# Performance work log

Hardware: AMD Instinct MI355X
Metric: run time of the kernel (lower is better)

## Reference

```python
import jax
import jax.numpy as jnp
import numpy as np

B, L = 64, 128


def _lse(x, axis):
    # -inf-safe logsumexp; mirrors the torch code's NaN-masking autograd hooks
    m = jax.lax.stop_gradient(jnp.max(x, axis=axis, keepdims=True))
    m = jnp.where(jnp.isfinite(m), m, 0.0)
    s = jnp.sum(jnp.exp(x - m), axis=axis)
    out = jnp.log(jnp.where(s > 0, s, 1.0)) + jnp.squeeze(m, axis=axis)
    return jnp.where(s > 0, out, -jnp.inf)


def _inside(scores_p, lens):
    # scores_p: [L, L, B] == torch scores.permute(2, 1, 0); Eisner inside algorithm
    L_, _, Bn = scores_p.shape
    ar = jnp.arange(L_)
    ninf = jnp.array(-jnp.inf, scores_p.dtype)
    s_i = jnp.full((L_, L_, Bn), -jnp.inf, scores_p.dtype)  # incomplete spans
    s_c = jnp.full((L_, L_, Bn), -jnp.inf, scores_p.dtype)  # complete spans
    s_c = s_c.at[ar, ar].set(0.0)

    def step(carry, w):
        s_i, s_c = carry
        i = ar[:, None]                      # span start
        j = ar[None, :]                      # split offset
        valid = (j < w) & (i < L_ - w)       # [L, L] stripe mask for width w
        clip = lambda x: jnp.clip(x, 0, L_ - 1)
        vi = (ar < L_ - w)[:, None]          # valid span starts, [L, 1]
        lo, hi = clip(ar + w), ar            # diagonal coords (i+w, i)

        # incomplete: I(i<->i+w) = lse_r C(i, i+r) + C(i+w, i+r+1)  (stripe + stripe(w,1))
        ilr = s_c[clip(i), clip(i + j)] + s_c[clip(i + w), clip(i + j + 1)]
        il = _lse(jnp.where(valid[..., None], ilr, ninf), 1)       # [L, B]
        s_i = s_i.at[lo, hi].set(jnp.where(vi, il + scores_p[lo, hi], s_i[lo, hi]))
        s_i = s_i.at[hi, lo].set(jnp.where(vi, il + scores_p[hi, lo], s_i[hi, lo]))

        # complete left: C(i+w -> i) = lse_r C(i+r, i) + I(i+w, i+r)
        cl = s_c[clip(i + j), clip(i)] + s_i[clip(i + w), clip(i + j)]
        clv = _lse(jnp.where(valid[..., None], cl, ninf), 1)
        s_c = s_c.at[lo, hi].set(jnp.where(vi, clv, s_c[lo, hi]))

        # complete right: C(i -> i+w) = lse_r I(i, i+r+1) + C(i+r+1, i+w)
        cr = s_i[clip(i), clip(i + j + 1)] + s_c[clip(i + j + 1), clip(i + w)]
        crv = _lse(jnp.where(valid[..., None], cr, ninf), 1)
        # root span (0, w) is only valid for sentences of exactly length w
        crv = crv.at[0].set(jnp.where(lens == w, crv[0], ninf))
        s_c = s_c.at[hi, lo].set(jnp.where(vi, crv, s_c[hi, lo]))
        return (s_i, s_c), None

    (s_i, s_c), _ = jax.lax.scan(jax.checkpoint(step), (s_i, s_c), jnp.arange(1, L_))
    return s_i, s_c


def setup_inputs() -> dict:
    key = jax.random.key(0)
    k1, k2, k3 = jax.random.split(key, 3)
    scores = jax.random.normal(k1, (B, L, L), jnp.float32)
    lens = jax.random.randint(k2, (B,), L // 2, L)                 # sentence lengths
    pos = jnp.arange(L)
    mask = (pos[None, :] >= 1) & (pos[None, :] <= lens[:, None])   # prefix mask, mask.sum(1)==lens
    target = jax.random.randint(k3, (B, L), 0, L)
    target = jnp.minimum(target, lens[:, None])                    # gold heads inside sentence
    return {"scores": scores, "mask": mask, "target": target}


def reference(scores, mask, target):
    Bn, L_, _ = scores.shape
    lens = mask.sum(1)
    total = mask.sum().astype(scores.dtype)
    s_i, s_c = _inside(jnp.transpose(scores, (2, 1, 0)), lens)
    logZ = s_c[0, lens, jnp.arange(Bn)].sum()
    gold = jnp.take_along_axis(scores, target[..., None], axis=-1)[..., 0]
    loss = (logZ - jnp.where(mask, gold, jnp.zeros((), scores.dtype)).sum()) / total
    return loss
```

## Files before the change

kernel.cpp:

```cpp
#include <hip/hip_runtime.h>
#include <math.h>

#define LL 128
#define LP 129
#define TCR 144
#define TC_SZ (TCR * LP)
#define TI_SZ (LL * LP + 160)
#define NT 512
#define NW 8

#define LOG2E 1.4426950408889634f
#define LN2   0.6931471805599453f

template <int CTRL>
__device__ __forceinline__ float dppq(float v) {
  return __int_as_float(__builtin_amdgcn_update_dpp(
      0, __float_as_int(v), CTRL, 0xF, 0xF, true));
}
__device__ __forceinline__ float qmax(float v) {
  v = fmaxf(v, dppq<0xB1>(v));
  v = fmaxf(v, dppq<0x4E>(v));
  return v;
}
__device__ __forceinline__ float qsum(float v) {
  v += dppq<0xB1>(v);
  v += dppq<0x4E>(v);
  return v;
}
template <int MASK>
__device__ __forceinline__ float swz(float v) {
  return __int_as_float(__builtin_amdgcn_ds_swizzle(
      __float_as_int(v), (MASK << 10) | 0x1F));
}
template <int G>
__device__ __forceinline__ float gmaxr(float v) {
  v = qmax(v);
  if constexpr (G >= 8)  v = fmaxf(v, swz<4>(v));
  if constexpr (G >= 16) v = fmaxf(v, swz<8>(v));
  if constexpr (G >= 32) v = fmaxf(v, swz<16>(v));
  return v;
}
template <int G>
__device__ __forceinline__ float gsumr(float v) {
  v = qsum(v);
  if constexpr (G >= 8)  v += swz<4>(v);
  if constexpr (G >= 16) v += swz<8>(v);
  if constexpr (G >= 32) v += swz<16>(v);
  return v;
}

template <int K>
__device__ __forceinline__ void fusedPhase(
    float* __restrict__ tC, float* __restrict__ tI, const float* __restrict__ S,
    const int ii, const int w, const int jg, const bool writer,
    const bool rootBad, float (&paR)[17], float (&a1R)[17], float (&c1R)[17]) {
  const float sUp = S[ii * LL + ii + w];
  const float sLo = S[(ii + w) * LL + ii];
  const float* pb = tC + (ii + w) * LP + ii + 1 + jg;
  const float* a2 = tI + (ii + w) * LP + ii + jg;
  const float* c2 = tC + (ii + 1 + jg) * LP + ii + w;

  float vb[K], va[K], vc[K];
#pragma unroll
  for (int k = 0; k < K; ++k) vb[k] = pb[4 * k];
#pragma unroll
  for (int k = 0; k < K; ++k) va[k] = a2[4 * k];
#pragma unroll
  for (int k = 0; k < K; ++k) vc[k] = c2[4 * k * LP];

  float mA0 = -INFINITY, mA1 = -INFINITY;
#pragma unroll
  for (int k = 0; k < K; ++k) {
    float x = paR[k] + vb[k];
    if (k & 1) mA1 = fmaxf(mA1, x); else mA0 = fmaxf(mA0, x);
  }
  const float msA = fmaxf(qmax(fmaxf(mA0, mA1)), -1e37f);
  const float nA = -msA * LOG2E;
  float sA0 = 0.f, sA1 = 0.f;
#pragma unroll
  for (int k = 0; k < K; ++k) {
    float e = __builtin_amdgcn_exp2f(__builtin_fmaf(paR[k] + vb[k], LOG2E, nA));
    if (k & 1) sA1 += e; else sA0 += e;
  }
  const float il = __builtin_amdgcn_logf(qsum(sA0 + sA1)) * LN2 + msA;

  float mL0 = -INFINITY, mL1 = -INFINITY;
#pragma unroll
  for (int k = 0; k < K; ++k) {
    float x = a1R[k] + va[k];
    if (k & 1) mL1 = fmaxf(mL1, x); else mL0 = fmaxf(mL0, x);
  }
  const float mL = qmax(fmaxf(mL0, mL1));
  const float msL = fmaxf(mL, -1e37f);
  const float nL = -msL * LOG2E;
  float sL0 = 0.f, sL1 = 0.f;
#pragma unroll
  for (int k = 0; k < K; ++k) {
    float e = __builtin_amdgcn_exp2f(__builtin_fmaf(a1R[k] + va[k], LOG2E, nL));
    if (k & 1) sL1 += e; else sL0 += e;
  }
  const float SL = qsum(sL0 + sL1);

  float mR0 = -INFINITY, mR1 = -INFINITY;
#pragma unroll
  for (int k = 0; k < K; ++k) {
    float x = c1R[k] + vc[k];
    if (k & 1) mR1 = fmaxf(mR1, x); else mR0 = fmaxf(mR0, x);
  }
  const float mR = qmax(fmaxf(mR0, mR1));
  const float msR = fmaxf(mR, -1e37f);
  const float nR = -msR * LOG2E;
  float sR0 = 0.f, sR1 = 0.f;
#pragma unroll
  for (int k = 0; k < K; ++k) {
    float e = __builtin_amdgcn_exp2f(__builtin_fmaf(c1R[k] + vc[k], LOG2E, nR));
    if (k & 1) sR1 += e; else sR0 += e;
  }
  const float SR = qsum(sR0 + sR1);

  const float t0 = il + sUp;
  const float tW = il + sLo;
  const float msfL = fmaxf(fmaxf(mL, t0), -1e37f);
  const float SLf = SL * __builtin_amdgcn_exp2f((msL - msfL) * LOG2E)
                  + __builtin_amdgcn_exp2f((t0 - msfL) * LOG2E);
  const float clv = __builtin_amdgcn_logf(SLf) * LN2 + msfL;
  const float msfR = fmaxf(fmaxf(mR, tW), -1e37f);
  const float SRf = SR * __builtin_amdgcn_exp2f((msR - msfR) * LOG2E)
                  + __builtin_amdgcn_exp2f((tW - msfR) * LOG2E);
  float crv = __builtin_amdgcn_logf(SRf) * LN2 + msfR;
  if (rootBad) crv = -INFINITY;

  if (writer) {
    tI[(ii + w) * LP + ii] = t0;
    tI[ii * LP + (ii + w)] = tW;
    tC[(ii + w) * LP + ii] = clv;
    tC[ii * LP + (ii + w)] = crv;
  }

  const int wm3 = w & 3;
  const bool lnw = (jg == wm3) && (wm3 != 0);
  paR[K - 1] = lnw ? crv : paR[K - 1];
  a1R[K - 1] = lnw ? clv : a1R[K - 1];
  if constexpr (K < 16) {
    const bool z = (jg == 0) && (wm3 == 0);
    paR[K] = z ? crv : paR[K];
    a1R[K] = z ? clv : a1R[K];
  } else {
    const bool z = (jg == 0) && (wm3 == 0);
    paR[16] = z ? crv : paR[16];
    a1R[16] = z ? clv : a1R[16];
  }
  const bool ln1 = (jg == ((w - 1) & 3));
  c1R[K - 1] = ln1 ? tW : c1R[K - 1];
}

template <int G, int KG>
__device__ __forceinline__ void widePhase(
    float* __restrict__ tC, float* __restrict__ tI, const float* __restrict__ S,
    const int ii, const int w, const int jgg, const bool writer,
    const bool rootBad) {
  const float sUp = S[ii * LL + ii + w];
  const float sLo = S[(ii + w) * LL + ii];
  const float* pa = tC + ii * LP + ii + jgg;
  const float* pb = tC + (ii + w) * LP + ii + 1 + jgg;
  const float* a1 = tC + (ii + jgg) * LP + ii;
  const float* a2 = tI + (ii + w) * LP + ii + jgg;
  const float* c1 = tI + ii * LP + ii + 1 + jgg;
  const float* c2 = tC + (ii + 1 + jgg) * LP + ii + w;

  float xa[KG], xl[KG], xr[KG];
  const unsigned uw = (unsigned)w, uw1 = (unsigned)(w - 1);
#pragma unroll
  for (int k = 0; k < KG; ++k) {
    float va_ = pa[G * k] + pb[G * k];
    float vl_ = a1[G * k * LP] + a2[G * k];
    float vr_ = c1[G * k] + c2[G * k * LP];
    const unsigned j = (unsigned)(jgg + G * k);
    xa[k] = (j < uw) ? va_ : -INFINITY;
    xl[k] = (j - 1u < uw1) ? vl_ : -INFINITY;
    xr[k] = (j < uw1) ? vr_ : -INFINITY;
  }

  float mA0 = -INFINITY, mA1 = -INFINITY;
#pragma unroll
  for (int k = 0; k < KG; ++k) {
    if (k & 1) mA1 = fmaxf(mA1, xa[k]); else mA0 = fmaxf(mA0, xa[k]);
  }
  const float msA = fmaxf(gmaxr<G>(fmaxf(mA0, mA1)), -1e37f);
  const float nA = -msA * LOG2E;
  float sA0 = 0.f, sA1 = 0.f;
#pragma unroll
  for (int k = 0; k < KG; ++k) {
    float e = __builtin_amdgcn_exp2f(__builtin_fmaf(xa[k], LOG2E, nA));
    if (k & 1) sA1 += e; else sA0 += e;
  }
  const float il = __builtin_amdgcn_logf(gsumr<G>(sA0 + sA1)) * LN2 + msA;

  float mL0 = -INFINITY, mL1 = -INFINITY;
#pragma unroll
  for (int k = 0; k < KG; ++k) {
    if (k & 1) mL1 = fmaxf(mL1, xl[k]); else mL0 = fmaxf(mL0, xl[k]);
  }
  const float mL = gmaxr<G>(fmaxf(mL0, mL1));
  const float msL = fmaxf(mL, -1e37f);
  const float nL = -msL * LOG2E;
  float sL0 = 0.f, sL1 = 0.f;
#pragma unroll
  for (int k = 0; k < KG; ++k) {
    float e = __builtin_amdgcn_exp2f(__builtin_fmaf(xl[k], LOG2E, nL));
    if (k & 1) sL1 += e; else sL0 += e;
  }
  const float SL = gsumr<G>(sL0 + sL1);

  float mR0 = -INFINITY, mR1 = -INFINITY;
#pragma unroll
  for (int k = 0; k < KG; ++k) {
    if (k & 1) mR1 = fmaxf(mR1, xr[k]); else mR0 = fmaxf(mR0, xr[k]);
  }
  const float mR = gmaxr<G>(fmaxf(mR0, mR1));
  const float msR = fmaxf(mR, -1e37f);
  const float nR = -msR * LOG2E;
  float sR0 = 0.f, sR1 = 0.f;
#pragma unroll
  for (int k = 0; k < KG; ++k) {
    float e = __builtin_amdgcn_exp2f(__builtin_fmaf(xr[k], LOG2E, nR));
    if (k & 1) sR1 += e; else sR0 += e;
  }
  const float SR = gsumr<G>(sR0 + sR1);

  const float t0 = il + sUp;
  const float tW = il + sLo;
  const float msfL = fmaxf(fmaxf(mL, t0), -1e37f);
  const float SLf = SL * __builtin_amdgcn_exp2f((msL - msfL) * LOG2E)
                  + __builtin_amdgcn_exp2f((t0 - msfL) * LOG2E);
  const float clv = __builtin_amdgcn_logf(SLf) * LN2 + msfL;
  const float msfR = fmaxf(fmaxf(mR, tW), -1e37f);
  const float SRf = SR * __builtin_amdgcn_exp2f((msR - msfR) * LOG2E)
                  + __builtin_amdgcn_exp2f((tW - msfR) * LOG2E);
  float crv = __builtin_amdgcn_logf(SRf) * LN2 + msfR;
  if (rootBad) crv = -INFINITY;

  if (writer) {
    tI[(ii + w) * LP + ii] = t0;
    tI[ii * LP + (ii + w)] = tW;
    tC[(ii + w) * LP + ii] = clv;
    tC[ii * LP + (ii + w)] = crv;
  }
}

__global__ __launch_bounds__(NT, 2) void crf_inside(
    const float* __restrict__ scores, const int* __restrict__ mask,
    const int* __restrict__ target, float* __restrict__ acc) {
  extern __shared__ float lds[];
  float* tC = lds;
  float* tI = lds + TC_SZ;
  const int b = blockIdx.x;
  const int t = threadIdx.x;
  const int lane = t & 63;
  const int wv = t >> 6;
  const int r = lane >> 2;
  const int jg = lane & 3;
  const float* S = scores + (size_t)b * LL * LL;

  __shared__ float gred[NW];
  __shared__ int lred[NW];
  __shared__ float s_gold;
  __shared__ int s_len;

  int mv = 0; float gv = 0.f;
  if (t < LL) {
    mv = mask[b * LL + t] ? 1 : 0;
    if (mv) gv = S[t * LL + target[b * LL + t]];
  }
  int lm = mv; float lg = gv;
#pragma unroll
  for (int o = 32; o > 0; o >>= 1) {
    lm += __shfl_xor(lm, o, 64);
    lg += __shfl_xor(lg, o, 64);
  }
  if (lane == 0) { lred[wv] = lm; gred[wv] = lg; }

  for (int idx = t; idx < TC_SZ + TI_SZ; idx += NT) lds[idx] = -INFINITY;
  __syncthreads();
  if (t < LL) tC[t * LP + t] = 0.f;
  if (t == 0) {
    int l = 0; float g = 0.f;
    for (int k = 0; k < NW; ++k) { l += lred[k]; g += gred[k]; }
    s_len = l; s_gold = g;
  }
  __syncthreads();
  const int len = s_len;

  const int i = (wv << 4) + r;

  float paR[17], a1R[17], c1R[17];
#pragma unroll
  for (int k = 0; k < 17; ++k) { paR[k] = -INFINITY; a1R[k] = -INFINITY; c1R[k] = -INFINITY; }
  if (jg == 0) paR[0] = 0.f;

  for (int w = 1; w <= 64; ++w) {
    const int ni = LL - w;
    const bool waveAct = (wv << 4) < ni;
    const int ii = min(i, ni - 1);
    const bool writer = (jg == 0) & (i < ni);
    const bool rootBad = (ii == 0) && (w != len);
    const int K = (w + 3) >> 2;
    if (waveAct) {
      switch (K) {
#define CASE_K(KK) case KK: fusedPhase<KK>(tC, tI, S, ii, w, jg, writer, rootBad, paR, a1R, c1R); break;
        CASE_K(1) CASE_K(2) CASE_K(3) CASE_K(4) CASE_K(5) CASE_K(6)
        CASE_K(7) CASE_K(8) CASE_K(9) CASE_K(10) CASE_K(11) CASE_K(12)
        CASE_K(13) CASE_K(14) CASE_K(15) CASE_K(16)
#undef CASE_K
      }
    }
    __syncthreads();
  }

  for (int w = 65; w < LL; ++w) {
    const int ni = LL - w;
    if (w <= 96) {
      const int gi = t >> 3, jgg = t & 7;
      if ((wv << 3) < ni) {
        const int ii = min(gi, ni - 1);
        const bool writer = (jgg == 0) & (gi < ni);
        const bool rootBad = (ii == 0) && (w != len);
        switch ((w + 7) >> 3) {
          case 9:  widePhase<8, 9>(tC, tI, S, ii, w, jgg, writer, rootBad); break;
          case 10: widePhase<8, 10>(tC, tI, S, ii, w, jgg, writer, rootBad); break;
          case 11: widePhase<8, 11>(tC, tI, S, ii, w, jgg, writer, rootBad); break;
          default: widePhase<8, 12>(tC, tI, S, ii, w, jgg, writer, rootBad); break;
        }
      }
    } else if (w <= 112) {
      const int gi = t >> 4, jgg = t & 15;
      if ((wv << 2) < ni) {
        const int ii = min(gi, ni - 1);
        const bool writer = (jgg == 0) & (gi < ni);
        const bool rootBad = (ii == 0) && (w != len);
        widePhase<16, 7>(tC, tI, S, ii, w, jgg, writer, rootBad);
      }
    } else {
      const int gi = t >> 5, jgg = t & 31;
      if ((wv << 1) < ni) {
        const int ii = min(gi, ni - 1);
        const bool writer = (jgg == 0) & (gi < ni);
        const bool rootBad = (ii == 0) && (w != len);
        widePhase<32, 4>(tC, tI, S, ii, w, jgg, writer, rootBad);
      }
    }
    __syncthreads();
  }

  if (t == 0) {
    float logZ = tC[len];
    atomicAdd(&acc[0], logZ - s_gold);
    atomicAdd(&acc[1], (float)len);
  }
}

__global__ void zero_acc(float* acc) {
  acc[0] = 0.f;
  acc[1] = 0.f;
}

__global__ void finalize(const float* __restrict__ acc, float* __restrict__ out) {
  out[0] = acc[0] / acc[1];
}

extern "C" void kernel_launch(void* const* d_in, const int* in_sizes, int n_in,
                              void* d_out, int out_size, void* d_ws, size_t ws_size,
                              hipStream_t stream) {
  const float* scores = (const float*)d_in[0];
  const int* mask = (const int*)d_in[1];
  const int* target = (const int*)d_in[2];
  float* out = (float*)d_out;
  float* acc = (float*)d_ws;

  const int Bn = in_sizes[0] / (LL * LL);
  const size_t lds_bytes = (size_t)(TC_SZ + TI_SZ) * sizeof(float);

  (void)hipFuncSetAttribute((const void*)crf_inside,
                            hipFuncAttributeMaxDynamicSharedMemorySize,
                            (int)lds_bytes);

  zero_acc<<<1, 1, 0, stream>>>(acc);
  crf_inside<<<Bn, NT, lds_bytes, stream>>>(scores, mask, target, acc);
  finalize<<<1, 1, 0, stream>>>(acc, out);
}
```

Measured before the change: 267.6 us.

## Double block to 1024 threads with 8-lane span groups and wider reductions

```diff
diff --git a/kernel.cpp b/kernel.cpp
--- a/kernel.cpp
+++ b/kernel.cpp
@@ -2,12 +2,12 @@
 #include <math.h>
 
 #define LL 128
-#define LP 129
-#define TCR 144
+#define LP 132
+#define TCR 160
 #define TC_SZ (TCR * LP)
-#define TI_SZ (LL * LP + 160)
-#define NT 512
-#define NW 8
+#define TI_SZ (LL * LP + 48)
+#define NT 1024
+#define NW 16
 
 #define LOG2E 1.4426950408889634f
 #define LN2   0.6931471805599453f
@@ -17,24 +17,27 @@
   return __int_as_float(__builtin_amdgcn_update_dpp(
       0, __float_as_int(v), CTRL, 0xF, 0xF, true));
 }
-__device__ __forceinline__ float qmax(float v) {
-  v = fmaxf(v, dppq<0xB1>(v));
-  v = fmaxf(v, dppq<0x4E>(v));
-  return v;
-}
-__device__ __forceinline__ float qsum(float v) {
-  v += dppq<0xB1>(v);
-  v += dppq<0x4E>(v);
-  return v;
-}
 template <int MASK>
 __device__ __forceinline__ float swz(float v) {
   return __int_as_float(__builtin_amdgcn_ds_swizzle(
       __float_as_int(v), (MASK << 10) | 0x1F));
 }
+__device__ __forceinline__ float g8max(float v) {
+  v = fmaxf(v, dppq<0xB1>(v));
+  v = fmaxf(v, dppq<0x4E>(v));
+  v = fmaxf(v, dppq<0x141>(v));
+  return v;
+}
+__device__ __forceinline__ float g8sum(float v) {
+  v += dppq<0xB1>(v);
+  v += dppq<0x4E>(v);
+  v += dppq<0x141>(v);
+  return v;
+}
 template <int G>
 __device__ __forceinline__ float gmaxr(float v) {
-  v = qmax(v);
+  v = fmaxf(v, dppq<0xB1>(v));
+  v = fmaxf(v, dppq<0x4E>(v));
   if constexpr (G >= 8)  v = fmaxf(v, swz<4>(v));
   if constexpr (G >= 16) v = fmaxf(v, swz<8>(v));
   if constexpr (G >= 32) v = fmaxf(v, swz<16>(v));
@@ -42,7 +45,8 @@
 }
 template <int G>
 __device__ __forceinline__ float gsumr(float v) {
-  v = qsum(v);
+  v += dppq<0xB1>(v);
+  v += dppq<0x4E>(v);
   if constexpr (G >= 8)  v += swz<4>(v);
   if constexpr (G >= 16) v += swz<8>(v);
   if constexpr (G >= 32) v += swz<16>(v);
@@ -52,21 +56,20 @@
 template <int K>
 __device__ __forceinline__ void fusedPhase(
     float* __restrict__ tC, float* __restrict__ tI, const float* __restrict__ S,
-    const int ii, const int w, const int jg, const bool writer,
-    const bool rootBad, float (&paR)[17], float (&a1R)[17], float (&c1R)[17]) {
+    const int ii, const int w, const int lg, const bool writer,
+    const bool rootBad, float (&paR)[9], float (&a1R)[9], float (&c1R)[8]) {
   const float sUp = S[ii * LL + ii + w];
   const float sLo = S[(ii + w) * LL + ii];
-  const float* pb = tC + (ii + w) * LP + ii + 1 + jg;
-  const float* a2 = tI + (ii + w) * LP + ii + jg;
-  const float* c2 = tC + (ii + 1 + jg) * LP + ii + w;
-
-  float vb[K], va[K], vc[K];
-#pragma unroll
-  for (int k = 0; k < K; ++k) vb[k] = pb[4 * k];
-#pragma unroll
-  for (int k = 0; k < K; ++k) va[k] = a2[4 * k];
-#pragma unroll
-  for (int k = 0; k < K; ++k) vc[k] = c2[4 * k * LP];
+  const float* pb = tC + (ii + w) * LP + ii + 1 + lg;
+  const float* a2 = tI + (ii + w) * LP + ii + lg;
+  const float* c2 = tC + (ii + 1 + lg) * LP + ii + w;
+
+  float vb[K], va[K];
+#pragma unroll
+  for (int k = 0; k < K; ++k) vb[k] = pb[8 * k];
+#pragma unroll
+  for (int k = 0; k < K; ++k) va[k] = a2[8 * k];
+  __builtin_amdgcn_sched_barrier(0);
 
   float mA0 = -INFINITY, mA1 = -INFINITY;
 #pragma unroll
@@ -74,7 +77,7 @@
     float x = paR[k] + vb[k];
     if (k & 1) mA1 = fmaxf(mA1, x); else mA0 = fmaxf(mA0, x);
   }
-  const float msA = fmaxf(qmax(fmaxf(mA0, mA1)), -1e37f);
+  const float msA = fmaxf(g8max(fmaxf(mA0, mA1)), -1e37f);
   const float nA = -msA * LOG2E;
   float sA0 = 0.f, sA1 = 0.f;
 #pragma unroll
@@ -82,7 +85,7 @@
     float e = __builtin_amdgcn_exp2f(__builtin_fmaf(paR[k] + vb[k], LOG2E, nA));
     if (k & 1) sA1 += e; else sA0 += e;
   }
-  const float il = __builtin_amdgcn_logf(qsum(sA0 + sA1)) * LN2 + msA;
+  const float il = __builtin_amdgcn_logf(g8sum(sA0 + sA1)) * LN2 + msA;
 
   float mL0 = -INFINITY, mL1 = -INFINITY;
 #pragma unroll
@@ -90,7 +93,7 @@
     float x = a1R[k] + va[k];
     if (k & 1) mL1 = fmaxf(mL1, x); else mL0 = fmaxf(mL0, x);
   }
-  const float mL = qmax(fmaxf(mL0, mL1));
+  const float mL = g8max(fmaxf(mL0, mL1));
   const float msL = fmaxf(mL, -1e37f);
   const float nL = -msL * LOG2E;
   float sL0 = 0.f, sL1 = 0.f;
@@ -99,7 +102,12 @@
     float e = __builtin_amdgcn_exp2f(__builtin_fmaf(a1R[k] + va[k], LOG2E, nL));
     if (k & 1) sL1 += e; else sL0 += e;
   }
-  const float SL = qsum(sL0 + sL1);
+  const float SL = g8sum(sL0 + sL1);
+
+  float vc[K];
+#pragma unroll
+  for (int k = 0; k < K; ++k) vc[k] = c2[8 * k * LP];
+  __builtin_amdgcn_sched_barrier(0);
 
   float mR0 = -INFINITY, mR1 = -INFINITY;
 #pragma unroll
@@ -107,7 +115,7 @@
     float x = c1R[k] + vc[k];
     if (k & 1) mR1 = fmaxf(mR1, x); else mR0 = fmaxf(mR0, x);
   }
-  const float mR = qmax(fmaxf(mR0, mR1));
+  const float mR = g8max(fmaxf(mR0, mR1));
   const float msR = fmaxf(mR, -1e37f);
   const float nR = -msR * LOG2E;
   float sR0 = 0.f, sR1 = 0.f;
@@ -116,7 +124,7 @@
     float e = __builtin_amdgcn_exp2f(__builtin_fmaf(c1R[k] + vc[k], LOG2E, nR));
     if (k & 1) sR1 += e; else sR0 += e;
   }
-  const float SR = qsum(sR0 + sR1);
+  const float SR = g8sum(sR0 + sR1);
 
   const float t0 = il + sUp;
   const float tW = il + sLo;
@@ -137,20 +145,16 @@
     tC[ii * LP + (ii + w)] = crv;
   }
 
-  const int wm3 = w & 3;
-  const bool lnw = (jg == wm3) && (wm3 != 0);
+  const int wm7 = w & 7;
+  const bool lnw = (lg == wm7) && (wm7 != 0);
   paR[K - 1] = lnw ? crv : paR[K - 1];
   a1R[K - 1] = lnw ? clv : a1R[K - 1];
-  if constexpr (K < 16) {
-    const bool z = (jg == 0) && (wm3 == 0);
+  {
+    const bool z = (lg == 0) && (wm7 == 0);
     paR[K] = z ? crv : paR[K];
     a1R[K] = z ? clv : a1R[K];
-  } else {
-    const bool z = (jg == 0) && (wm3 == 0);
-    paR[16] = z ? crv : paR[16];
-    a1R[16] = z ? clv : a1R[16];
-  }
-  const bool ln1 = (jg == ((w - 1) & 3));
+  }
+  const bool ln1 = (lg == ((w - 1) & 7));
   c1R[K - 1] = ln1 ? tW : c1R[K - 1];
 }
 
@@ -248,7 +252,9 @@
   }
 }
 
-__global__ __launch_bounds__(NT, 2) void crf_inside(
+__global__ __launch_bounds__(NT)
+__attribute__((amdgpu_waves_per_eu(4, 4)))
+void crf_inside(
     const float* __restrict__ scores, const int* __restrict__ mask,
     const int* __restrict__ target, float* __restrict__ acc) {
   extern __shared__ float lds[];
@@ -258,8 +264,8 @@
   const int t = threadIdx.x;
   const int lane = t & 63;
   const int wv = t >> 6;
-  const int r = lane >> 2;
-  const int jg = lane & 3;
+  const int g = t >> 3;
+  const int lg = t & 7;
   const float* S = scores + (size_t)b * LL * LL;
 
   __shared__ float gred[NW];
@@ -272,82 +278,70 @@
     mv = mask[b * LL + t] ? 1 : 0;
     if (mv) gv = S[t * LL + target[b * LL + t]];
   }
-  int lm = mv; float lg = gv;
+  int lm = mv; float lg_ = gv;
 #pragma unroll
   for (int o = 32; o > 0; o >>= 1) {
     lm += __shfl_xor(lm, o, 64);
-    lg += __shfl_xor(lg, o, 64);
-  }
-  if (lane == 0) { lred[wv] = lm; gred[wv] = lg; }
+    lg_ += __shfl_xor(lg_, o, 64);
+  }
+  if (lane == 0) { lred[wv] = lm; gred[wv] = lg_; }
 
   for (int idx = t; idx < TC_SZ + TI_SZ; idx += NT) lds[idx] = -INFINITY;
   __syncthreads();
   if (t < LL) tC[t * LP + t] = 0.f;
   if (t == 0) {
-    int l = 0; float g = 0.f;
-    for (int k = 0; k < NW; ++k) { l += lred[k]; g += gred[k]; }
-    s_len = l; s_gold = g;
+    int l = 0; float gg = 0.f;
+    for (int k = 0; k < NW; ++k) { l += lred[k]; gg += gred[k]; }
+    s_len = l; s_gold = gg;
   }
   __syncthreads();
   const int len = s_len;
 
-  const int i = (wv << 4) + r;
-
-  float paR[17], a1R[17], c1R[17];
-#pragma unroll
-  for (int k = 0; k < 17; ++k) { paR[k] = -INFINITY; a1R[k] = -INFINITY; c1R[k] = -INFINITY; }
-  if (jg == 0) paR[0] = 0.f;
+  float paR[9], a1R[9], c1R[8];
+#pragma unroll
+  for (int k = 0; k < 9; ++k) { paR[k] = -INFINITY; a1R[k] = -INFINITY; }
+#pragma unroll
+  for (int k = 0; k < 8; ++k) c1R[k] = -INFINITY;
+  if (lg == 0) paR[0] = 0.f;
 
   for (int w = 1; w <= 64; ++w) {
     const int ni = LL - w;
-    const bool waveAct = (wv << 4) < ni;
-    const int ii = min(i, ni - 1);
-    const bool writer = (jg == 0) & (i < ni);
+    const bool waveAct = (wv << 3) < ni;
+    const int ii = min(g, ni - 1);
+    const bool writer = (lg == 0) & (g < ni);
     const bool rootBad = (ii == 0) && (w != len);
-    const int K = (w + 3) >> 2;
+    const int K = (w + 7) >> 3;
     if (waveAct) {
       switch (K) {
-#define CASE_K(KK) case KK: fusedPhase<KK>(tC, tI, S, ii, w, jg, writer, rootBad, paR, a1R, c1R); break;
-        CASE_K(1) CASE_K(2) CASE_K(3) CASE_K(4) CASE_K(5) CASE_K(6)
-        CASE_K(7) CASE_K(8) CASE_K(9) CASE_K(10) CASE_K(11) CASE_K(12)
-        CASE_K(13) CASE_K(14) CASE_K(15) CASE_K(16)
+#define CASE_K(KK) case KK: fusedPhase<KK>(tC, tI, S, ii, w, lg, writer, rootBad, paR, a1R, c1R); break;
+        CASE_K(1) CASE_K(2) CASE_K(3) CASE_K(4)
+        CASE_K(5) CASE_K(6) CASE_K(7) CASE_K(8)
 #undef CASE_K
       }
     }
     __syncthreads();
   }
 
-  for (int w = 65; w < LL; ++w) {
+  for (int w = 65; w <= 96; ++w) {
     const int ni = LL - w;
-    if (w <= 96) {
-      const int gi = t >> 3, jgg = t & 7;
-      if ((wv << 3) < ni) {
-        const int ii = min(gi, ni - 1);
-        const bool writer = (jgg == 0) & (gi < ni);
-        const bool rootBad = (ii == 0) && (w != len);
-        switch ((w + 7) >> 3) {
-          case 9:  widePhase<8, 9>(tC, tI, S, ii, w, jgg, writer, rootBad); break;
-          case 10: widePhase<8, 10>(tC, tI, S, ii, w, jgg, writer, rootBad); break;
-          case 11: widePhase<8, 11>(tC, tI, S, ii, w, jgg, writer, rootBad); break;
-          default: widePhase<8, 12>(tC, tI, S, ii, w, jgg, writer, rootBad); break;
-        }
-      }
-    } else if (w <= 112) {
-      const int gi = t >> 4, jgg = t & 15;
-      if ((wv << 2) < ni) {
-        const int ii = min(gi, ni - 1);
-        const bool writer = (jgg == 0) & (gi < ni);
-        const bool rootBad = (ii == 0) && (w != len);
-        widePhase<16, 7>(tC, tI, S, ii, w, jgg, writer, rootBad);
-      }
-    } else {
-      const int gi = t >> 5, jgg = t & 31;
-      if ((wv << 1) < ni) {
-        const int ii = min(gi, ni - 1);
-        const bool writer = (jgg == 0) & (gi < ni);
-        const bool rootBad = (ii == 0) && (w != len);
-        widePhase<32, 4>(tC, tI, S, ii, w, jgg, writer, rootBad);
-      }
+    const int gi = t >> 4, jgg = t & 15;
+    if ((wv << 2) < ni) {
+      const int ii = min(gi, ni - 1);
+      const bool writer = (jgg == 0) & (gi < ni);
+      const bool rootBad = (ii == 0) && (w != len);
+      widePhase<16, 6>(tC, tI, S, ii, w, jgg, writer, rootBad);
+    }
+    __syncthreads();
+  }
+
+  for (int w = 97; w < LL; ++w) {
+    const int ni = LL - w;
+    const int gi = t >> 5, jgg = t & 31;
+    if ((wv << 1) < ni) {
+      const int ii = min(gi, ni - 1);
+      const bool writer = (jgg == 0) & (gi < ni);
+      const bool rootBad = (ii == 0) && (w != len);
+      widePhase<32, 4>(tC, tI, S, ii, w, jgg, writer, rootBad);
     }
     __syncthreads();
   }
```

Measured after the change: 253.6 us. 1.06x faster.
